# Kernel optimization log

Measured on AMD Instinct MI355X. Metric: run time of the kernel, lower is better.

Reference implementation:

```python
import jax, jax.numpy as jnp
import numpy as np

P = 16  # num_partitions
DIN = 256  # in_features // P
DOUT = 256  # out_features // P

def setup_inputs() -> dict:
    key = jax.random.key(0)
    k1, k2, k3 = jax.random.split(key, 3)
    inputs = jax.random.normal(k1, (8, 2048, P * DIN), dtype=jnp.float32)
    weight = jax.random.normal(k2, (P, DOUT, DIN), dtype=jnp.float32) * (1.0 / np.sqrt(DIN))
    bias = jax.random.normal(k3, (P * DOUT,), dtype=jnp.float32) * (1.0 / np.sqrt(DIN))
    return {"inputs": inputs, "weight": weight, "bias": bias}

def reference(inputs, weight, bias):
    # inputs: (B, S, P*DIN) -> (B, S, P, DIN)
    x = inputs.reshape(*inputs.shape[:-1], P, DIN)
    # block-diagonal matmul: (B,S,P,DIN) x (P,DOUT,DIN) -> (B,S,P,DOUT)
    y = jnp.einsum('bspi,poi->bspo', x, weight)
    # transpose=True: swap (P, DOUT) -> (DOUT, P), then flatten
    y = jnp.swapaxes(y, -2, -1)
    y = y.reshape(*y.shape[:-2], DOUT * P)
    return y + bias
```

## Files before the change

kernel.cpp:

```cpp
#include <hip/hip_runtime.h>


typedef __attribute__((ext_vector_type(4))) float f32x4;
typedef __attribute__((ext_vector_type(8))) short short8;

#define SLICE_STRIDE 1040
#define BUF_BYTES    (16 * SLICE_STRIDE)
#define NBUF         4
#define LDS_TOTAL    (NBUF * BUF_BYTES)

__device__ __forceinline__ unsigned int pk2(float a, float b) {
  union { float f; unsigned int u; } x, y;
  x.f = a; y.f = b;
  unsigned int ua = x.u + (0x7fffu + ((x.u >> 16) & 1u));
  unsigned int ub = y.u + (0x7fffu + ((y.u >> 16) & 1u));
  return (ua >> 16) | (ub & 0xffff0000u);
}

__device__ __forceinline__ unsigned int cvtpk(float a, float b) {
  unsigned int r;
  asm("v_cvt_pk_bf16_f32 %0, %1, %2" : "=v"(r) : "v"(a), "v"(b));
  return r;
}

__device__ __forceinline__ void dma_row(const float* g, char* l) {
  __builtin_amdgcn_global_load_lds(
      (const __attribute__((address_space(1))) unsigned int*)g,
      (__attribute__((address_space(3))) unsigned int*)l, 16, 0, 0);
}

__global__ __launch_bounds__(256) void wconv_kernel(
    const float* __restrict__ w, unsigned int* __restrict__ o) {
  int i = blockIdx.x * 256 + threadIdx.x;
  float4 f = ((const float4*)w)[i];
  uint2 u;
  u.x = pk2(f.x, f.y);
  u.y = pk2(f.z, f.w);
  ((uint2*)o)[i] = u;
}

__global__ __launch_bounds__(256, 2) void diag_gemm_kernel(
    const float* __restrict__ x, const unsigned short* __restrict__ wb,
    const float* __restrict__ bias, float* __restrict__ out) {
  extern __shared__ char lds[];
  const int tid = threadIdx.x;
  const int wv  = tid >> 6;
  const int l   = tid & 63;
  const long T0 = (long)blockIdx.x * 16;

  const int n  = l & 15;
  const int kg = l >> 4;

  const int C0 = (wv * 16 + n) * 256 + kg * 8;
  const float* xrow0 = x + (T0 + wv * 4) * 4096 + l * 4;

  short8 a[8], b[2][8];

#pragma unroll
  for (int sl = 0; sl < 3; ++sl) {
#pragma unroll
    for (int i = 0; i < 4; ++i)
      dma_row(xrow0 + i * 4096 + sl * 256,
              lds + sl * BUF_BYTES + (wv * 4 + i) * SLICE_STRIDE);
  }
  __builtin_amdgcn_sched_barrier(0);
  {
    const unsigned short* bp = wb + C0;
#pragma unroll
    for (int ks = 0; ks < 8; ++ks) b[0][ks] = *(const short8*)(bp + ks * 32);
  }
  __builtin_amdgcn_sched_barrier(0);
  asm volatile("s_waitcnt vmcnt(16)" ::: "memory");
  __builtin_amdgcn_s_barrier();
  __builtin_amdgcn_sched_barrier(0);

  float* obase = out + T0 * 4096;

  for (int s = 0; s < 4; ++s) {
    f32x4 res[16];
#pragma unroll
    for (int p = 0; p < 16; ++p) {
      const int cur = p & 1, nxt = cur ^ 1;

      const char* ab = lds + (p & 3) * BUF_BYTES + n * SLICE_STRIDE + kg * 32;
#pragma unroll
      for (int ks = 0; ks < 8; ++ks) {
        f32x4 lo = *(const f32x4*)(ab + ks * 128);
        f32x4 hi = *(const f32x4*)(ab + ks * 128 + 16);
        union { unsigned int u[4]; short8 s8; } t;
        t.u[0] = cvtpk(lo[0], lo[1]);
        t.u[1] = cvtpk(lo[2], lo[3]);
        t.u[2] = cvtpk(hi[0], hi[1]);
        t.u[3] = cvtpk(hi[2], hi[3]);
        a[ks] = t.s8;
      }

      if (p != 15) {
        const unsigned short* bp = wb + C0 + s * 16384 + (p + 1) * 65536;
#pragma unroll
        for (int ks = 0; ks < 8; ++ks) b[nxt][ks] = *(const short8*)(bp + ks * 32);
      } else if (s != 3) {
        const unsigned short* bp = wb + C0 + (s + 1) * 16384;
#pragma unroll
        for (int ks = 0; ks < 8; ++ks) b[nxt][ks] = *(const short8*)(bp + ks * 32);
      }

      if (p < 13 || s != 3) {
        const int p3 = (p + 3) & 15;
#pragma unroll
        for (int i = 0; i < 4; ++i)
          dma_row(xrow0 + i * 4096 + p3 * 256,
                  lds + ((p + 3) & 3) * BUF_BYTES + (wv * 4 + i) * SLICE_STRIDE);
      }

      f32x4 acc = {0.f, 0.f, 0.f, 0.f};
#pragma unroll
      for (int ks = 0; ks < 8; ++ks)
        acc = __builtin_amdgcn_mfma_f32_16x16x32_bf16(a[ks], b[cur][ks], acc, 0, 0, 0);
      res[p] = acc;

      if (!(p == 15 && s == 3)) {
        __builtin_amdgcn_sched_barrier(0);
        if (p == 13 && s == 3)      asm volatile("s_waitcnt vmcnt(12)" ::: "memory");
        else if (p == 14 && s == 3) asm volatile("s_waitcnt vmcnt(8)"  ::: "memory");
        else                        asm volatile("s_waitcnt vmcnt(16)" ::: "memory");
        __builtin_amdgcn_s_barrier();
        __builtin_amdgcn_sched_barrier(0);
      }
    }

    const int o0 = (wv + 4 * s) * 16;
    const float* bp2 = bias + (o0 + n) * 16;
    float4 bv0 = ((const float4*)bp2)[0];
    float4 bv1 = ((const float4*)bp2)[1];
    float4 bv2 = ((const float4*)bp2)[2];
    float4 bv3 = ((const float4*)bp2)[3];
    float* ob = obase + (long)(o0 + n) * 16;
#pragma unroll
    for (int r = 0; r < 4; ++r) {
      float* orow = ob + (long)(kg * 4 + r) * 4096;
      float4 v0 = make_float4(res[0][r] + bv0.x, res[1][r] + bv0.y,
                              res[2][r] + bv0.z, res[3][r] + bv0.w);
      float4 v1 = make_float4(res[4][r] + bv1.x, res[5][r] + bv1.y,
                              res[6][r] + bv1.z, res[7][r] + bv1.w);
      float4 v2 = make_float4(res[8][r] + bv2.x, res[9][r] + bv2.y,
                              res[10][r] + bv2.z, res[11][r] + bv2.w);
      float4 v3 = make_float4(res[12][r] + bv3.x, res[13][r] + bv3.y,
                              res[14][r] + bv3.z, res[15][r] + bv3.w);
      ((float4*)orow)[0] = v0;
      ((float4*)orow)[1] = v1;
      ((float4*)orow)[2] = v2;
      ((float4*)orow)[3] = v3;
    }
  }
}

extern "C" void kernel_launch(void* const* d_in, const int* in_sizes, int n_in,
                              void* d_out, int out_size, void* d_ws, size_t ws_size,
                              hipStream_t stream) {
  const float* x    = (const float*)d_in[0];
  const float* w    = (const float*)d_in[1];
  const float* bias = (const float*)d_in[2];
  float* out = (float*)d_out;
  unsigned int* wb = (unsigned int*)d_ws;

  (void)hipFuncSetAttribute((const void*)diag_gemm_kernel,
                            hipFuncAttributeMaxDynamicSharedMemorySize, LDS_TOTAL);

  wconv_kernel<<<1024, 256, 0, stream>>>(w, wb);

  diag_gemm_kernel<<<1024, 256, LDS_TOTAL, stream>>>(
      x, (const unsigned short*)wb, bias, out);
}
```

Before: 719.1 us.

## Use 512-thread blocks so each wave covers two output tiles in one pass

The block grows from 4 to 8 waves. Each wave now computes two 16-column output groups per partition, so each 16-token tile is walked over the 16 partitions once instead of four times. Each wave issues half as many x rows to LDS, and the bf16 conversion of the A operand from LDS is done once per slice instead of being repeated across four output passes. The cost is more accumulator registers (32 f32x4), no double buffering of the weight loads, and a larger block that may lower occupancy under launch_bounds(512,2).

```diff
diff --git a/kernel.cpp b/kernel.cpp
--- a/kernel.cpp
+++ b/kernel.cpp
@@ -39,7 +39,7 @@
   ((uint2*)o)[i] = u;
 }
 
-__global__ __launch_bounds__(256, 2) void diag_gemm_kernel(
+__global__ __launch_bounds__(512, 2) void diag_gemm_kernel(
     const float* __restrict__ x, const unsigned short* __restrict__ wb,
     const float* __restrict__ bias, float* __restrict__ out) {
   extern __shared__ char lds[];
@@ -51,85 +51,80 @@
   const int n  = l & 15;
   const int kg = l >> 4;
 
-  const int C0 = (wv * 16 + n) * 256 + kg * 8;
-  const float* xrow0 = x + (T0 + wv * 4) * 4096 + l * 4;
+  const float* xdma = x + (T0 + wv * 2) * 4096 + l * 4;
 
-  short8 a[8], b[2][8];
+  const unsigned short* b0base = wb + (wv * 16 + n) * 256 + kg * 8;
+  const unsigned short* b1base = wb + ((wv + 8) * 16 + n) * 256 + kg * 8;
+
+  short8 a[8], b0[8], b1[8];
+  f32x4 res[2][16];
 
 #pragma unroll
   for (int sl = 0; sl < 3; ++sl) {
-#pragma unroll
-    for (int i = 0; i < 4; ++i)
-      dma_row(xrow0 + i * 4096 + sl * 256,
-              lds + sl * BUF_BYTES + (wv * 4 + i) * SLICE_STRIDE);
+    dma_row(xdma + sl * 256,        lds + sl * BUF_BYTES + (wv * 2) * SLICE_STRIDE);
+    dma_row(xdma + 4096 + sl * 256, lds + sl * BUF_BYTES + (wv * 2 + 1) * SLICE_STRIDE);
   }
   __builtin_amdgcn_sched_barrier(0);
-  {
-    const unsigned short* bp = wb + C0;
-#pragma unroll
-    for (int ks = 0; ks < 8; ++ks) b[0][ks] = *(const short8*)(bp + ks * 32);
-  }
-  __builtin_amdgcn_sched_barrier(0);
-  asm volatile("s_waitcnt vmcnt(16)" ::: "memory");
+  asm volatile("s_waitcnt vmcnt(4)" ::: "memory");
   __builtin_amdgcn_s_barrier();
   __builtin_amdgcn_sched_barrier(0);
 
+#pragma unroll
+  for (int p = 0; p < 16; ++p) {
+    const unsigned short* bp0 = b0base + p * 65536;
+    const unsigned short* bp1 = b1base + p * 65536;
+#pragma unroll
+    for (int ks = 0; ks < 8; ++ks) b0[ks] = *(const short8*)(bp0 + ks * 32);
+#pragma unroll
+    for (int ks = 0; ks < 8; ++ks) b1[ks] = *(const short8*)(bp1 + ks * 32);
+    __builtin_amdgcn_sched_barrier(0);
+
+    const char* ab = lds + (p & 3) * BUF_BYTES + n * SLICE_STRIDE + kg * 32;
+#pragma unroll
+    for (int ks = 0; ks < 8; ++ks) {
+      f32x4 lo = *(const f32x4*)(ab + ks * 128);
+      f32x4 hi = *(const f32x4*)(ab + ks * 128 + 16);
+      union { unsigned int u[4]; short8 s8; } t;
+      t.u[0] = cvtpk(lo[0], lo[1]);
+      t.u[1] = cvtpk(lo[2], lo[3]);
+      t.u[2] = cvtpk(hi[0], hi[1]);
+      t.u[3] = cvtpk(hi[2], hi[3]);
+      a[ks] = t.s8;
+    }
+    __builtin_amdgcn_sched_barrier(0);
+
+    if (p < 13) {
+      dma_row(xdma + (p + 3) * 256,
+              lds + ((p + 3) & 3) * BUF_BYTES + (wv * 2) * SLICE_STRIDE);
+      dma_row(xdma + 4096 + (p + 3) * 256,
+              lds + ((p + 3) & 3) * BUF_BYTES + (wv * 2 + 1) * SLICE_STRIDE);
+    }
+    __builtin_amdgcn_sched_barrier(0);
+
+    f32x4 acc0 = (f32x4){0.f, 0.f, 0.f, 0.f};
+    f32x4 acc1 = (f32x4){0.f, 0.f, 0.f, 0.f};
+#pragma unroll
+    for (int ks = 0; ks < 8; ++ks)
+      acc0 = __builtin_amdgcn_mfma_f32_16x16x32_bf16(a[ks], b0[ks], acc0, 0, 0, 0);
+#pragma unroll
+    for (int ks = 0; ks < 8; ++ks)
+      acc1 = __builtin_amdgcn_mfma_f32_16x16x32_bf16(a[ks], b1[ks], acc1, 0, 0, 0);
+    res[0][p] = acc0;
+    res[1][p] = acc1;
+
+    if (p < 15) {
+      __builtin_amdgcn_sched_barrier(0);
+      if (p < 13) asm volatile("s_waitcnt vmcnt(2)" ::: "memory");
+      else        asm volatile("s_waitcnt vmcnt(0)" ::: "memory");
+      __builtin_amdgcn_s_barrier();
+      __builtin_amdgcn_sched_barrier(0);
+    }
+  }
+
   float* obase = out + T0 * 4096;
-
-  for (int s = 0; s < 4; ++s) {
-    f32x4 res[16];
 #pragma unroll
-    for (int p = 0; p < 16; ++p) {
-      const int cur = p & 1, nxt = cur ^ 1;
-
-      const char* ab = lds + (p & 3) * BUF_BYTES + n * SLICE_STRIDE + kg * 32;
-#pragma unroll
-      for (int ks = 0; ks < 8; ++ks) {
-        f32x4 lo = *(const f32x4*)(ab + ks * 128);
-        f32x4 hi = *(const f32x4*)(ab + ks * 128 + 16);
-        union { unsigned int u[4]; short8 s8; } t;
-        t.u[0] = cvtpk(lo[0], lo[1]);
-        t.u[1] = cvtpk(lo[2], lo[3]);
-        t.u[2] = cvtpk(hi[0], hi[1]);
-        t.u[3] = cvtpk(hi[2], hi[3]);
-        a[ks] = t.s8;
-      }
-
-      if (p != 15) {
-        const unsigned short* bp = wb + C0 + s * 16384 + (p + 1) * 65536;
-#pragma unroll
-        for (int ks = 0; ks < 8; ++ks) b[nxt][ks] = *(const short8*)(bp + ks * 32);
-      } else if (s != 3) {
-        const unsigned short* bp = wb + C0 + (s + 1) * 16384;
-#pragma unroll
-        for (int ks = 0; ks < 8; ++ks) b[nxt][ks] = *(const short8*)(bp + ks * 32);
-      }
-
-      if (p < 13 || s != 3) {
-        const int p3 = (p + 3) & 15;
-#pragma unroll
-        for (int i = 0; i < 4; ++i)
-          dma_row(xrow0 + i * 4096 + p3 * 256,
-                  lds + ((p + 3) & 3) * BUF_BYTES + (wv * 4 + i) * SLICE_STRIDE);
-      }
-
-      f32x4 acc = {0.f, 0.f, 0.f, 0.f};
-#pragma unroll
-      for (int ks = 0; ks < 8; ++ks)
-        acc = __builtin_amdgcn_mfma_f32_16x16x32_bf16(a[ks], b[cur][ks], acc, 0, 0, 0);
-      res[p] = acc;
-
-      if (!(p == 15 && s == 3)) {
-        __builtin_amdgcn_sched_barrier(0);
-        if (p == 13 && s == 3)      asm volatile("s_waitcnt vmcnt(12)" ::: "memory");
-        else if (p == 14 && s == 3) asm volatile("s_waitcnt vmcnt(8)"  ::: "memory");
-        else                        asm volatile("s_waitcnt vmcnt(16)" ::: "memory");
-        __builtin_amdgcn_s_barrier();
-        __builtin_amdgcn_sched_barrier(0);
-      }
-    }
-
-    const int o0 = (wv + 4 * s) * 16;
+  for (int s = 0; s < 2; ++s) {
+    const int o0 = (wv + 8 * s) * 16;
     const float* bp2 = bias + (o0 + n) * 16;
     float4 bv0 = ((const float4*)bp2)[0];
     float4 bv1 = ((const float4*)bp2)[1];
@@ -139,14 +134,14 @@
 #pragma unroll
     for (int r = 0; r < 4; ++r) {
       float* orow = ob + (long)(kg * 4 + r) * 4096;
-      float4 v0 = make_float4(res[0][r] + bv0.x, res[1][r] + bv0.y,
-                              res[2][r] + bv0.z, res[3][r] + bv0.w);
-      float4 v1 = make_float4(res[4][r] + bv1.x, res[5][r] + bv1.y,
-                              res[6][r] + bv1.z, res[7][r] + bv1.w);
-      float4 v2 = make_float4(res[8][r] + bv2.x, res[9][r] + bv2.y,
-                              res[10][r] + bv2.z, res[11][r] + bv2.w);
-      float4 v3 = make_float4(res[12][r] + bv3.x, res[13][r] + bv3.y,
-                              res[14][r] + bv3.z, res[15][r] + bv3.w);
+      float4 v0 = make_float4(res[s][0][r] + bv0.x, res[s][1][r] + bv0.y,
+                              res[s][2][r] + bv0.z, res[s][3][r] + bv0.w);
+      float4 v1 = make_float4(res[s][4][r] + bv1.x, res[s][5][r] + bv1.y,
+                              res[s][6][r] + bv1.z, res[s][7][r] + bv1.w);
+      float4 v2 = make_float4(res[s][8][r] + bv2.x, res[s][9][r] + bv2.y,
+                              res[s][10][r] + bv2.z, res[s][11][r] + bv2.w);
+      float4 v3 = make_float4(res[s][12][r] + bv3.x, res[s][13][r] + bv3.y,
+                              res[s][14][r] + bv3.z, res[s][15][r] + bv3.w);
       ((float4*)orow)[0] = v0;
       ((float4*)orow)[1] = v1;
       ((float4*)orow)[2] = v2;
@@ -169,6 +164,6 @@
 
   wconv_kernel<<<1024, 256, 0, stream>>>(w, wb);
 
-  diag_gemm_kernel<<<1024, 256, LDS_TOTAL, stream>>>(
+  diag_gemm_kernel<<<1024, 512, LDS_TOTAL, stream>>>(
       x, (const unsigned short*)wb, bias, out);
 }
```

Result: faster. 662.9 us (-7.8%).

## Split output strips across blocks with XCD-aware block remapping and triple buffering

Applied to the files above, without the earlier changes.

Each block now computes one 16-token by 64-output strip instead of all four strips, launching four times as many blocks. Block indices are remapped so the four blocks sharing the same input rows land on the same XCD to reuse input rows via L2. LDS buffering drops from four to three slices and launch bounds allow three blocks per CU for higher occupancy. The cost is re-reading each input slice up to four times from cache/HBM and losing the weight-register double buffering.

```diff
diff --git a/kernel.cpp b/kernel.cpp
--- a/kernel.cpp
+++ b/kernel.cpp
@@ -6,7 +6,7 @@
 
 #define SLICE_STRIDE 1040
 #define BUF_BYTES    (16 * SLICE_STRIDE)
-#define NBUF         4
+#define NBUF         3
 #define LDS_TOTAL    (NBUF * BUF_BYTES)
 
 __device__ __forceinline__ unsigned int pk2(float a, float b) {
@@ -39,119 +39,109 @@
   ((uint2*)o)[i] = u;
 }
 
-__global__ __launch_bounds__(256, 2) void diag_gemm_kernel(
+__global__ __launch_bounds__(256, 3) void diag_gemm_kernel(
     const float* __restrict__ x, const unsigned short* __restrict__ wb,
     const float* __restrict__ bias, float* __restrict__ out) {
   extern __shared__ char lds[];
   const int tid = threadIdx.x;
   const int wv  = tid >> 6;
   const int l   = tid & 63;
-  const long T0 = (long)blockIdx.x * 16;
+
+  const int d = blockIdx.x;
+  const int w = (d & 7) * 512 + (d >> 3);
+  const int g  = w >> 2;
+  const int sb = w & 3;
+  const long T0 = (long)g * 16;
 
   const int n  = l & 15;
   const int kg = l >> 4;
 
-  const int C0 = (wv * 16 + n) * 256 + kg * 8;
-  const float* xrow0 = x + (T0 + wv * 4) * 4096 + l * 4;
+  const int strip = sb * 4 + wv;
+  const unsigned short* bbase = wb + (strip * 16 + n) * 256 + kg * 8;
+  const float* xdma = x + (T0 + wv * 4) * 4096 + l * 4;
 
-  short8 a[8], b[2][8];
+  short8 a[8], b[8];
+  f32x4 res[16];
 
 #pragma unroll
-  for (int sl = 0; sl < 3; ++sl) {
+  for (int sl = 0; sl < 2; ++sl) {
 #pragma unroll
     for (int i = 0; i < 4; ++i)
-      dma_row(xrow0 + i * 4096 + sl * 256,
+      dma_row(xdma + i * 4096 + sl * 256,
               lds + sl * BUF_BYTES + (wv * 4 + i) * SLICE_STRIDE);
   }
   __builtin_amdgcn_sched_barrier(0);
-  {
-    const unsigned short* bp = wb + C0;
-#pragma unroll
-    for (int ks = 0; ks < 8; ++ks) b[0][ks] = *(const short8*)(bp + ks * 32);
-  }
-  __builtin_amdgcn_sched_barrier(0);
-  asm volatile("s_waitcnt vmcnt(16)" ::: "memory");
+  asm volatile("s_waitcnt vmcnt(4)" ::: "memory");
   __builtin_amdgcn_s_barrier();
   __builtin_amdgcn_sched_barrier(0);
 
+#pragma unroll
+  for (int p = 0; p < 16; ++p) {
+    const unsigned short* bp = bbase + p * 65536;
+#pragma unroll
+    for (int ks = 0; ks < 8; ++ks) b[ks] = *(const short8*)(bp + ks * 32);
+    __builtin_amdgcn_sched_barrier(0);
+
+    const char* ab = lds + (p % 3) * BUF_BYTES + n * SLICE_STRIDE + kg * 32;
+#pragma unroll
+    for (int ks = 0; ks < 8; ++ks) {
+      f32x4 lo = *(const f32x4*)(ab + ks * 128);
+      f32x4 hi = *(const f32x4*)(ab + ks * 128 + 16);
+      union { unsigned int u[4]; short8 s8; } t;
+      t.u[0] = cvtpk(lo[0], lo[1]);
+      t.u[1] = cvtpk(lo[2], lo[3]);
+      t.u[2] = cvtpk(hi[0], hi[1]);
+      t.u[3] = cvtpk(hi[2], hi[3]);
+      a[ks] = t.s8;
+    }
+    __builtin_amdgcn_sched_barrier(0);
+
+    if (p < 14) {
+#pragma unroll
+      for (int i = 0; i < 4; ++i)
+        dma_row(xdma + i * 4096 + (p + 2) * 256,
+                lds + ((p + 2) % 3) * BUF_BYTES + (wv * 4 + i) * SLICE_STRIDE);
+    }
+    __builtin_amdgcn_sched_barrier(0);
+
+    f32x4 acc = (f32x4){0.f, 0.f, 0.f, 0.f};
+#pragma unroll
+    for (int ks = 0; ks < 8; ++ks)
+      acc = __builtin_amdgcn_mfma_f32_16x16x32_bf16(a[ks], b[ks], acc, 0, 0, 0);
+    res[p] = acc;
+
+    if (p < 15) {
+      __builtin_amdgcn_sched_barrier(0);
+      if (p < 14) asm volatile("s_waitcnt vmcnt(4)" ::: "memory");
+      else        asm volatile("s_waitcnt vmcnt(0)" ::: "memory");
+      __builtin_amdgcn_s_barrier();
+      __builtin_amdgcn_sched_barrier(0);
+    }
+  }
+
+  const int o0 = strip * 16;
   float* obase = out + T0 * 4096;
-
-  for (int s = 0; s < 4; ++s) {
-    f32x4 res[16];
+  const float* bp2 = bias + (o0 + n) * 16;
+  float4 bv0 = ((const float4*)bp2)[0];
+  float4 bv1 = ((const float4*)bp2)[1];
+  float4 bv2 = ((const float4*)bp2)[2];
+  float4 bv3 = ((const float4*)bp2)[3];
+  float* ob = obase + (long)(o0 + n) * 16;
 #pragma unroll
-    for (int p = 0; p < 16; ++p) {
-      const int cur = p & 1, nxt = cur ^ 1;
-
-      const char* ab = lds + (p & 3) * BUF_BYTES + n * SLICE_STRIDE + kg * 32;
-#pragma unroll
-      for (int ks = 0; ks < 8; ++ks) {
-        f32x4 lo = *(const f32x4*)(ab + ks * 128);
-        f32x4 hi = *(const f32x4*)(ab + ks * 128 + 16);
-        union { unsigned int u[4]; short8 s8; } t;
-        t.u[0] = cvtpk(lo[0], lo[1]);
-        t.u[1] = cvtpk(lo[2], lo[3]);
-        t.u[2] = cvtpk(hi[0], hi[1]);
-        t.u[3] = cvtpk(hi[2], hi[3]);
-        a[ks] = t.s8;
-      }
-
-      if (p != 15) {
-        const unsigned short* bp = wb + C0 + s * 16384 + (p + 1) * 65536;
-#pragma unroll
-        for (int ks = 0; ks < 8; ++ks) b[nxt][ks] = *(const short8*)(bp + ks * 32);
-      } else if (s != 3) {
-        const unsigned short* bp = wb + C0 + (s + 1) * 16384;
-#pragma unroll
-        for (int ks = 0; ks < 8; ++ks) b[nxt][ks] = *(const short8*)(bp + ks * 32);
-      }
-
-      if (p < 13 || s != 3) {
-        const int p3 = (p + 3) & 15;
-#pragma unroll
-        for (int i = 0; i < 4; ++i)
-          dma_row(xrow0 + i * 4096 + p3 * 256,
-                  lds + ((p + 3) & 3) * BUF_BYTES + (wv * 4 + i) * SLICE_STRIDE);
-      }
-
-      f32x4 acc = {0.f, 0.f, 0.f, 0.f};
-#pragma unroll
-      for (int ks = 0; ks < 8; ++ks)
-        acc = __builtin_amdgcn_mfma_f32_16x16x32_bf16(a[ks], b[cur][ks], acc, 0, 0, 0);
-      res[p] = acc;
-
-      if (!(p == 15 && s == 3)) {
-        __builtin_amdgcn_sched_barrier(0);
-        if (p == 13 && s == 3)      asm volatile("s_waitcnt vmcnt(12)" ::: "memory");
-        else if (p == 14 && s == 3) asm volatile("s_waitcnt vmcnt(8)"  ::: "memory");
-        else                        asm volatile("s_waitcnt vmcnt(16)" ::: "memory");
-        __builtin_amdgcn_s_barrier();
-        __builtin_amdgcn_sched_barrier(0);
-      }
-    }
-
-    const int o0 = (wv + 4 * s) * 16;
-    const float* bp2 = bias + (o0 + n) * 16;
-    float4 bv0 = ((const float4*)bp2)[0];
-    float4 bv1 = ((const float4*)bp2)[1];
-    float4 bv2 = ((const float4*)bp2)[2];
-    float4 bv3 = ((const float4*)bp2)[3];
-    float* ob = obase + (long)(o0 + n) * 16;
-#pragma unroll
-    for (int r = 0; r < 4; ++r) {
-      float* orow = ob + (long)(kg * 4 + r) * 4096;
-      float4 v0 = make_float4(res[0][r] + bv0.x, res[1][r] + bv0.y,
-                              res[2][r] + bv0.z, res[3][r] + bv0.w);
-      float4 v1 = make_float4(res[4][r] + bv1.x, res[5][r] + bv1.y,
-                              res[6][r] + bv1.z, res[7][r] + bv1.w);
-      float4 v2 = make_float4(res[8][r] + bv2.x, res[9][r] + bv2.y,
-                              res[10][r] + bv2.z, res[11][r] + bv2.w);
-      float4 v3 = make_float4(res[12][r] + bv3.x, res[13][r] + bv3.y,
-                              res[14][r] + bv3.z, res[15][r] + bv3.w);
-      ((float4*)orow)[0] = v0;
-      ((float4*)orow)[1] = v1;
-      ((float4*)orow)[2] = v2;
-      ((float4*)orow)[3] = v3;
-    }
+  for (int r = 0; r < 4; ++r) {
+    float* orow = ob + (long)(kg * 4 + r) * 4096;
+    float4 v0 = make_float4(res[0][r] + bv0.x, res[1][r] + bv0.y,
+                            res[2][r] + bv0.z, res[3][r] + bv0.w);
+    float4 v1 = make_float4(res[4][r] + bv1.x, res[5][r] + bv1.y,
+                            res[6][r] + bv1.z, res[7][r] + bv1.w);
+    float4 v2 = make_float4(res[8][r] + bv2.x, res[9][r] + bv2.y,
+                            res[10][r] + bv2.z, res[11][r] + bv2.w);
+    float4 v3 = make_float4(res[12][r] + bv3.x, res[13][r] + bv3.y,
+                            res[14][r] + bv3.z, res[15][r] + bv3.w);
+    ((float4*)orow)[0] = v0;
+    ((float4*)orow)[1] = v1;
+    ((float4*)orow)[2] = v2;
+    ((float4*)orow)[3] = v3;
   }
 }
 
@@ -169,6 +159,6 @@
 
   wconv_kernel<<<1024, 256, 0, stream>>>(w, wb);
 
-  diag_gemm_kernel<<<1024, 256, LDS_TOTAL, stream>>>(
+  diag_gemm_kernel<<<4096, 256, LDS_TOTAL, stream>>>(
       x, (const unsigned short*)wb, bias, out);
 }
```

After: 663.9 us. 7.7% less time.
